# Kernel optimization log

Measured on AMD Instinct MI355X. Metric: run time of the kernel, lower is better.

Reference implementation:

```python
import jax, jax.numpy as jnp
import numpy as np
from jax import lax

BETA = 0.95
THRESH = 1.0
NUM_STEPS = 50
NUM_IN, NUM_HID, NUM_OUT = 2, 64, 2
BATCH = 262144


def _heaviside(u):
    return (u > 0).astype(u.dtype)


def setup_inputs() -> dict:
    key = jax.random.key(0)
    k_x, k_w1, k_b1, k_w2, k_b2 = jax.random.split(key, 5)
    x = jax.random.uniform(k_x, (BATCH, NUM_IN), dtype=jnp.float32)
    # torch Linear default init: U(-1/sqrt(fan_in), 1/sqrt(fan_in))
    s1 = 1.0 / np.sqrt(NUM_IN)
    s2 = 1.0 / np.sqrt(NUM_HID)
    W1 = jax.random.uniform(k_w1, (NUM_HID, NUM_IN), jnp.float32, -s1, s1)
    b1 = jax.random.uniform(k_b1, (NUM_HID,), jnp.float32, -s1, s1)
    W2 = jax.random.uniform(k_w2, (NUM_OUT, NUM_HID), jnp.float32, -s2, s2)
    b2 = jax.random.uniform(k_b2, (NUM_OUT,), jnp.float32, -s2, s2)
    return {"x": x, "W1": W1, "b1": b1, "W2": W2, "b2": b2}


def reference(x, W1, b1, W2, b2):
    # cur1 is loop-invariant (same x fed every step)
    cur1 = x @ W1.T + b1  # [B, H]

    def step(carry, _):
        mem1, mem2 = carry
        # snntorch Leaky, reset_mechanism='subtract', threshold=1.0
        reset1 = _heaviside(mem1 - THRESH)
        mem1 = BETA * mem1 + cur1 - reset1 * THRESH
        spk1 = _heaviside(mem1 - THRESH)
        cur2 = spk1 @ W2.T + b2  # [B, O]
        reset2 = _heaviside(mem2 - THRESH)
        mem2 = BETA * mem2 + cur2 - reset2 * THRESH
        spk2 = _heaviside(mem2 - THRESH)
        return (mem1, mem2), (spk2, mem2)

    B = x.shape[0]
    mem1_0 = jnp.zeros((B, NUM_HID), x.dtype)
    mem2_0 = jnp.zeros((B, NUM_OUT), x.dtype)
    _, (spk2_rec, mem2_rec) = lax.scan(step, (mem1_0, mem2_0), None, length=NUM_STEPS)
    return spk2_rec, mem2_rec  # each [50, B, 2]
```

## Files before the change

### kernel.cpp

```cpp
#include <hip/hip_runtime.h>

#define BATCH 262144
#define HID 64
#define NSTEP 50

__global__ __launch_bounds__(256) void snn_fused(
    const float* __restrict__ x,
    const float* __restrict__ W1,
    const float* __restrict__ b1,
    const float* __restrict__ W2,
    const float* __restrict__ b2,
    float* __restrict__ out)
{
    const int b = blockIdx.x * 256 + threadIdx.x;
    const float2 xv = reinterpret_cast<const float2*>(x)[b];

    float acc0[NSTEP], acc1[NSTEP];
#pragma unroll
    for (int t = 0; t < NSTEP; ++t) { acc0[t] = 0.0f; acc1[t] = 0.0f; }

#pragma unroll 2
    for (int h = 0; h < HID; ++h) {
        const float w10 = W1[2 * h + 0];
        const float w11 = W1[2 * h + 1];
        const float w20 = W2[h];
        const float w21 = W2[HID + h];
        float c = __fmul_rn(xv.x, w10);
        c = __builtin_fmaf(xv.y, w11, c);
        const float cur = __fadd_rn(c, b1[h]);

        float m = 0.0f;
        float spk = 0.0f;
#pragma unroll
        for (int t = 0; t < NSTEP; ++t) {
            m = __fsub_rn(__fadd_rn(__fmul_rn(0.95f, m), cur), spk);
            spk = (m > 1.0f) ? 1.0f : 0.0f;
            acc0[t] = __builtin_fmaf(spk, w20, acc0[t]);
            acc1[t] = __builtin_fmaf(spk, w21, acc1[t]);
        }
    }

    const float bb0 = b2[0], bb1 = b2[1];
    float m0 = 0.0f, m1 = 0.0f, s0 = 0.0f, s1 = 0.0f;
    float2* outspk = reinterpret_cast<float2*>(out) + b;
    float2* outmem = reinterpret_cast<float2*>(out) + (size_t)NSTEP * BATCH + b;
#pragma unroll
    for (int t = 0; t < NSTEP; ++t) {
        const float c0 = __fadd_rn(acc0[t], bb0);
        const float c1 = __fadd_rn(acc1[t], bb1);
        m0 = __fsub_rn(__fadd_rn(__fmul_rn(0.95f, m0), c0), s0);
        m1 = __fsub_rn(__fadd_rn(__fmul_rn(0.95f, m1), c1), s1);
        s0 = (m0 > 1.0f) ? 1.0f : 0.0f;
        s1 = (m1 > 1.0f) ? 1.0f : 0.0f;
        outspk[(size_t)t * BATCH] = make_float2(s0, s1);
        outmem[(size_t)t * BATCH] = make_float2(m0, m1);
    }
}

extern "C" void kernel_launch(void* const* d_in, const int* in_sizes, int n_in,
                              void* d_out, int out_size, void* d_ws, size_t ws_size,
                              hipStream_t stream)
{
    const float* x  = (const float*)d_in[0];
    const float* W1 = (const float*)d_in[1];
    const float* b1 = (const float*)d_in[2];
    const float* W2 = (const float*)d_in[3];
    const float* b2 = (const float*)d_in[4];
    float* out = (float*)d_out;
    snn_fused<<<BATCH / 256, 256, 0, stream>>>(x, W1, b1, W2, b2, out);
}
```

Measured before the change: 128.0 us.

## Swap loop order to keep hidden state in registers, stream outputs per step

```diff
diff --git a/kernel.cpp b/kernel.cpp
--- a/kernel.cpp
+++ b/kernel.cpp
@@ -4,7 +4,7 @@
 #define HID 64
 #define NSTEP 50
 
-__global__ __launch_bounds__(256) void snn_fused(
+__global__ __launch_bounds__(256, 2) void snn_fused(
     const float* __restrict__ x,
     const float* __restrict__ W1,
     const float* __restrict__ b1,
@@ -15,39 +15,33 @@
     const int b = blockIdx.x * 256 + threadIdx.x;
     const float2 xv = reinterpret_cast<const float2*>(x)[b];
 
-    float acc0[NSTEP], acc1[NSTEP];
+    float cur[HID], m[HID], spk[HID];
 #pragma unroll
-    for (int t = 0; t < NSTEP; ++t) { acc0[t] = 0.0f; acc1[t] = 0.0f; }
-
-#pragma unroll 2
     for (int h = 0; h < HID; ++h) {
-        const float w10 = W1[2 * h + 0];
-        const float w11 = W1[2 * h + 1];
-        const float w20 = W2[h];
-        const float w21 = W2[HID + h];
-        float c = __fmul_rn(xv.x, w10);
-        c = __builtin_fmaf(xv.y, w11, c);
-        const float cur = __fadd_rn(c, b1[h]);
-
-        float m = 0.0f;
-        float spk = 0.0f;
-#pragma unroll
-        for (int t = 0; t < NSTEP; ++t) {
-            m = __fsub_rn(__fadd_rn(__fmul_rn(0.95f, m), cur), spk);
-            spk = (m > 1.0f) ? 1.0f : 0.0f;
-            acc0[t] = __builtin_fmaf(spk, w20, acc0[t]);
-            acc1[t] = __builtin_fmaf(spk, w21, acc1[t]);
-        }
+        float c = __fmul_rn(xv.x, W1[2 * h + 0]);
+        c = __builtin_fmaf(xv.y, W1[2 * h + 1], c);
+        cur[h] = __fadd_rn(c, b1[h]);
+        m[h] = 0.0f;
+        spk[h] = 0.0f;
     }
 
     const float bb0 = b2[0], bb1 = b2[1];
     float m0 = 0.0f, m1 = 0.0f, s0 = 0.0f, s1 = 0.0f;
     float2* outspk = reinterpret_cast<float2*>(out) + b;
     float2* outmem = reinterpret_cast<float2*>(out) + (size_t)NSTEP * BATCH + b;
+
+#pragma unroll 1
+    for (int t = 0; t < NSTEP; ++t) {
+        float a0 = 0.0f, a1 = 0.0f;
 #pragma unroll
-    for (int t = 0; t < NSTEP; ++t) {
-        const float c0 = __fadd_rn(acc0[t], bb0);
-        const float c1 = __fadd_rn(acc1[t], bb1);
+        for (int h = 0; h < HID; ++h) {
+            m[h] = __fsub_rn(__fadd_rn(__fmul_rn(0.95f, m[h]), cur[h]), spk[h]);
+            spk[h] = (m[h] > 1.0f) ? 1.0f : 0.0f;
+            a0 = __builtin_fmaf(spk[h], W2[h], a0);
+            a1 = __builtin_fmaf(spk[h], W2[HID + h], a1);
+        }
+        const float c0 = __fadd_rn(a0, bb0);
+        const float c1 = __fadd_rn(a1, bb1);
         m0 = __fsub_rn(__fadd_rn(__fmul_rn(0.95f, m0), c0), s0);
         m1 = __fsub_rn(__fadd_rn(__fmul_rn(0.95f, m1), c1), s1);
         s0 = (m0 > 1.0f) ? 1.0f : 0.0f;
```

Measured after the change: 129.2 us. Within noise of the previous version (+0.9%).
